# Performance work log

Measured on AMD Instinct MI355X. Metric: run time of the kernel, lower is better.

## Reference

```python
import jax, jax.numpy as jnp
import numpy as np

N_NODES = 50000


def _add_self_loops(src, dst, n):
    loop = jnp.arange(n, dtype=src.dtype)
    return jnp.concatenate([src, loop]), jnp.concatenate([dst, loop])


def gcn_conv(x, src, dst, W, b, n):
    # PyG GCNConv: out = D^-1/2 (A+I) D^-1/2 (x W) + b
    h = x @ W                                        # [N, out]
    deg = jnp.zeros((n,), h.dtype).at[dst].add(1.0)  # in-degree incl. self-loops
    dinv = jax.lax.rsqrt(jnp.maximum(deg, 1e-12))
    norm = dinv[src] * dinv[dst]                     # [E]
    msg = h[src] * norm[:, None]                     # [E, out] gather
    return jax.ops.segment_sum(msg, dst, num_segments=n) + b


def setup_inputs() -> dict:
    key = jax.random.key(0)
    ks = jax.random.split(key, 10)
    num_features, hidden = 256, 64
    x = jax.random.normal(ks[0], (N_NODES, num_features), jnp.float32)
    edge_index = jax.random.randint(ks[1], (2, 1600000), 0, N_NODES, jnp.int64)

    def glorot(k, fi, fo):
        s = jnp.sqrt(6.0 / (fi + fo)).astype(jnp.float32)
        return jax.random.uniform(k, (fi, fo), jnp.float32, -s, s)

    dims = [(num_features, 2 * hidden), (2 * hidden, hidden),
            (hidden, 2 * hidden), (2 * hidden, num_features)]
    params = {}
    for i, (fi, fo) in enumerate(dims):
        params[f"W{i+1}"] = glorot(ks[2 + i], fi, fo)
        params[f"b{i+1}"] = jnp.zeros((fo,), jnp.float32)
    return {"x": x, "edge_index": edge_index, **params}


def reference(x, edge_index, W1, b1, W2, b2, W3, b3, W4, b4):
    n = x.shape[0]
    src, dst = _add_self_loops(edge_index[0], edge_index[1], n)
    h = jax.nn.relu(gcn_conv(x, src, dst, W1, b1, n))
    z = jax.nn.relu(gcn_conv(h, src, dst, W2, b2, n))
    h = jax.nn.relu(gcn_conv(z, src, dst, W3, b3, n))
    x_hat = gcn_conv(h, src, dst, W4, b4, n)
    return x_hat
```

## Files before the change

### kernel.cpp

```cpp
#include <hip/hip_runtime.h>
#include <cstdint>
#include <cstddef>


static inline int cdiv(int a, int b) { return (a + b - 1) / b; }

typedef _Float16 half8v __attribute__((ext_vector_type(8)));
typedef float f32x4 __attribute__((ext_vector_type(4)));

#define NBMAX 784
#define SCHUNK 8192

__global__ __launch_bounds__(256) void k_bhist(const int* __restrict__ dst,
                                               int* __restrict__ bh,
                                               int E, int nb, int perBlock) {
  __shared__ int h[NBMAX];
  for (int i = threadIdx.x; i < nb; i += 256) h[i] = 0;
  __syncthreads();
  int beg = blockIdx.x * perBlock;
  int end = min(beg + perBlock, E);
  for (int e = beg + threadIdx.x; e < end; e += 256)
    atomicAdd(&h[dst[e] >> 6], 1);
  __syncthreads();
  for (int i = threadIdx.x; i < nb; i += 256)
    if (h[i]) atomicAdd(&bh[i], h[i]);
}

__global__ __launch_bounds__(256) void k_bscan(const int* __restrict__ bh,
                                               int* __restrict__ boff,
                                               int* __restrict__ bcur, int nb) {
  __shared__ int tsum[256];
  int t = threadIdx.x;
  int v[4];
  int s = 0;
#pragma unroll
  for (int i = 0; i < 4; ++i) {
    int idx = t * 4 + i;
    v[i] = (idx < nb) ? bh[idx] : 0;
    s += v[i];
  }
  tsum[t] = s;
  __syncthreads();
  int x = s;
  for (int d = 1; d < 256; d <<= 1) {
    int add = (t >= d) ? tsum[t - d] : 0;
    __syncthreads();
    x += add;
    tsum[t] = x;
    __syncthreads();
  }
  int base = x - s;
#pragma unroll
  for (int i = 0; i < 4; ++i) {
    int idx = t * 4 + i;
    if (idx < nb) { boff[idx] = base; bcur[idx] = base; }
    base += v[i];
  }
  if (t == 255) boff[nb] = base;
}

__global__ __launch_bounds__(256) void k_bscatter(const int* __restrict__ src,
                                                  const int* __restrict__ dst,
                                                  int* __restrict__ bcur,
                                                  unsigned* __restrict__ tmp,
                                                  int E, int nb) {
  __shared__ int hist[NBMAX];
  __shared__ int base[NBMAX];
  int beg = blockIdx.x * SCHUNK;
  int end = min(beg + SCHUNK, E);
  for (int i = threadIdx.x; i < nb; i += 256) hist[i] = 0;
  __syncthreads();
  for (int e = beg + threadIdx.x; e < end; e += 256)
    atomicAdd(&hist[dst[e] >> 6], 1);
  __syncthreads();
  for (int b = threadIdx.x; b < nb; b += 256) {
    int c = hist[b];
    base[b] = c ? atomicAdd(&bcur[b], c) : 0;
    hist[b] = 0;
  }
  __syncthreads();
  for (int e = beg + threadIdx.x; e < end; e += 256) {
    int d = dst[e];
    int b = d >> 6;
    int lp = atomicAdd(&hist[b], 1);
    tmp[base[b] + lp] = ((unsigned)(d & 63) << 16) | (unsigned)src[e];
  }
}

__global__ __launch_bounds__(256) void k_bsort(const unsigned* __restrict__ tmp,
                                               const int* __restrict__ boff,
                                               unsigned short* __restrict__ esrc,
                                               int* __restrict__ offs,
                                               int* __restrict__ counts,
                                               float* __restrict__ dinv,
                                               int N) {
  __shared__ int hist[64], cur[64];
  int b = blockIdx.x;
  int t = threadIdx.x;
  if (t < 64) hist[t] = 0;
  __syncthreads();
  int beg = boff[b], end = boff[b + 1];
  int cnt = end - beg;
  for (int i = t; i < cnt; i += 256) atomicAdd(&hist[tmp[beg + i] >> 16], 1);
  __syncthreads();
  if (t < 64) {
    int v = hist[t];
    int x = v;
#pragma unroll
    for (int d = 1; d < 64; d <<= 1) {
      int up = __shfl_up(x, d, 64);
      if (t >= d) x += up;
    }
    int ex = x - v;
    cur[t] = ex;
    int node = b * 64 + t;
    if (node < N) {
      counts[node] = v;
      offs[node] = beg + ex;
      dinv[node] = rsqrtf((float)(v + 1));
    }
  }
  __syncthreads();
  for (int i = t; i < cnt; i += 256) {
    unsigned v = tmp[beg + i];
    int pos = atomicAdd(&cur[v >> 16], 1);
    esrc[beg + pos] = (unsigned short)(v & 0xFFFFu);
  }
}

__global__ __launch_bounds__(256) void k_prepw(const float* __restrict__ W1,
                                               const float* __restrict__ W2,
                                               const float* __restrict__ W3,
                                               const float* __restrict__ W4,
                                               _Float16* __restrict__ W1t,
                                               _Float16* __restrict__ W2t,
                                               _Float16* __restrict__ W3t,
                                               _Float16* __restrict__ W4t,
                                               int* __restrict__ bh) {
  int t = blockIdx.x * 256 + threadIdx.x;
  if (t < NBMAX) bh[t] = 0;
  if (t < 32768) {
    int m = t >> 8, k = t & 255;
    W1t[t] = (_Float16)W1[k * 128 + m];
  } else if (t < 40960) {
    int u = t - 32768;
    int m = u >> 7, k = u & 127;
    W2t[u] = (_Float16)W2[k * 64 + m];
  } else if (t < 49152) {
    int u = t - 40960;
    int m = u >> 6, k = u & 63;
    W3t[u] = (_Float16)W3[k * 128 + m];
  } else if (t < 81920) {
    int u = t - 49152;
    int m = u >> 7, k = u & 127;
    W4t[u] = (_Float16)W4[k * 256 + m];
  }
}

template <int W, int BIAS, int RELU, int POST>
__global__ __launch_bounds__(256) void k_pull16(const _Float16* __restrict__ h,
                                                const unsigned short* __restrict__ esrc,
                                                const int* __restrict__ offs,
                                                const int* __restrict__ counts,
                                                const float* __restrict__ dinv,
                                                const float* __restrict__ bias,
                                                _Float16* __restrict__ out, int n) {
  const int LPR = W / 8;
  const int GRP = 64 / LPR;
  int node = blockIdx.x * 4 + (threadIdx.x >> 6);
  if (node >= n) return;
  int lane = threadIdx.x & 63;
  int g  = lane / LPR;
  int fl = lane % LPR;
  size_t rbase = (size_t)node * W + fl * 8;

  float acc[8] = {};
  if (g == 0) {
    half8v sv = *(const half8v*)&h[rbase];
#pragma unroll
    for (int q = 0; q < 8; ++q) acc[q] = (float)sv[q];
  }

  int beg = offs[node];
  int cnt = counts[node];
  int j = g;
  for (; j + 3 * GRP < cnt; j += 4 * GRP) {
    int s0 = esrc[beg + j];
    int s1 = esrc[beg + j + GRP];
    int s2 = esrc[beg + j + 2 * GRP];
    int s3 = esrc[beg + j + 3 * GRP];
    half8v v0 = *(const half8v*)&h[(size_t)s0 * W + fl * 8];
    half8v v1 = *(const half8v*)&h[(size_t)s1 * W + fl * 8];
    half8v v2 = *(const half8v*)&h[(size_t)s2 * W + fl * 8];
    half8v v3 = *(const half8v*)&h[(size_t)s3 * W + fl * 8];
#pragma unroll
    for (int q = 0; q < 8; ++q)
      acc[q] += ((float)v0[q] + (float)v1[q]) + ((float)v2[q] + (float)v3[q]);
  }
  for (; j < cnt; j += GRP) {
    int s = esrc[beg + j];
    half8v v = *(const half8v*)&h[(size_t)s * W + fl * 8];
#pragma unroll
    for (int q = 0; q < 8; ++q) acc[q] += (float)v[q];
  }

#pragma unroll
  for (int d = LPR; d < 64; d <<= 1) {
#pragma unroll
    for (int q = 0; q < 8; ++q) acc[q] += __shfl_xor(acc[q], d, 64);
  }

  if (g == 0) {
    float dv = dinv[node];
    float t[8];
#pragma unroll
    for (int q = 0; q < 8; ++q) t[q] = dv * acc[q];
    if (BIAS) {
#pragma unroll
      for (int q = 0; q < 8; ++q) t[q] += bias[fl * 8 + q];
    }
    if (RELU) {
#pragma unroll
      for (int q = 0; q < 8; ++q) t[q] = fmaxf(t[q], 0.f);
    }
    if (POST) {
#pragma unroll
      for (int q = 0; q < 8; ++q) t[q] *= dv;
    }
    half8v o;
#pragma unroll
    for (int q = 0; q < 8; ++q) o[q] = (_Float16)t[q];
    *(half8v*)&out[rbase] = o;
  }
}

template <int M, int K, int BIAS, int RELU, int SCALE, int AF32, int OUTF16>
__global__ __launch_bounds__(256) void k_gemm_mfma(const void* __restrict__ Av,
                                                   const _Float16* __restrict__ Wt,
                                                   const float* __restrict__ bias,
                                                   const float* __restrict__ dinv,
                                                   void* __restrict__ Cv, int N) {
  const int NT = M / 64;
  const int ST = K / 32;
  const int w  = threadIdx.x >> 6;
  const int l  = threadIdx.x & 63;
  const int lr = l & 15;
  const int lk = l >> 4;
  const int r0 = blockIdx.x * 16;
  int arow = r0 + lr;
  if (arow >= N) arow = N - 1;

  half8v a_all[ST];
  half8v b_all[ST][NT];

#pragma unroll
  for (int s = 0; s < ST; ++s) {
    int k0 = s * 32;
    if (AF32) {
      const float* ap = &((const float*)Av)[(size_t)arow * K + k0 + lk * 8];
      float4 f0 = *(const float4*)ap;
      float4 f1 = *(const float4*)(ap + 4);
      half8v a;
      a[0] = (_Float16)f0.x; a[1] = (_Float16)f0.y;
      a[2] = (_Float16)f0.z; a[3] = (_Float16)f0.w;
      a[4] = (_Float16)f1.x; a[5] = (_Float16)f1.y;
      a[6] = (_Float16)f1.z; a[7] = (_Float16)f1.w;
      a_all[s] = a;
    } else {
      a_all[s] = *(const half8v*)&((const _Float16*)Av)[(size_t)arow * K + k0 + lk * 8];
    }
#pragma unroll
    for (int ct = 0; ct < NT; ++ct) {
      int col0 = (w * NT + ct) * 16;
      b_all[s][ct] = *(const half8v*)&Wt[(size_t)(col0 + lr) * K + k0 + lk * 8];
    }
  }

  f32x4 acc[NT] = {};
#pragma unroll
  for (int s = 0; s < ST; ++s)
#pragma unroll
    for (int ct = 0; ct < NT; ++ct)
      acc[ct] = __builtin_amdgcn_mfma_f32_16x16x32_f16(a_all[s], b_all[s][ct], acc[ct], 0, 0, 0);

  float dvv[4];
  int okr[4];
#pragma unroll
  for (int r = 0; r < 4; ++r) {
    int ro = r0 + lk * 4 + r;
    okr[r] = (ro < N);
    dvv[r] = (SCALE && okr[r]) ? dinv[ro] : 1.0f;
  }
#pragma unroll
  for (int ct = 0; ct < NT; ++ct) {
    int col = (w * NT + ct) * 16 + lr;
    float bs = BIAS ? bias[col] : 0.f;
#pragma unroll
    for (int r = 0; r < 4; ++r) {
      if (!okr[r]) continue;
      int ro = r0 + lk * 4 + r;
      float v = acc[ct][r] + bs;
      if (RELU) v = fmaxf(v, 0.f);
      if (SCALE) v *= dvv[r];
      if (OUTF16) ((_Float16*)Cv)[(size_t)ro * M + col] = (_Float16)v;
      else        ((float*)Cv)[(size_t)ro * M + col] = v;
    }
  }
}

extern "C" void kernel_launch(void* const* d_in, const int* in_sizes, int n_in,
                              void* d_out, int out_size, void* d_ws, size_t ws_size,
                              hipStream_t stream) {
  const float* x  = (const float*)d_in[0];
  const int*   ei = (const int*)d_in[1];
  const float* W1 = (const float*)d_in[2];
  const float* b1 = (const float*)d_in[3];
  const float* W2 = (const float*)d_in[4];
  const float* b2 = (const float*)d_in[5];
  const float* W3 = (const float*)d_in[6];
  const float* b3 = (const float*)d_in[7];
  const float* W4 = (const float*)d_in[8];
  const float* b4 = (const float*)d_in[9];

  const int N = in_sizes[0] / 256;
  const int E = in_sizes[1] / 2;
  const int* src = ei;
  const int* dst = ei + E;
  const int nb = cdiv(N, 64);

  const int NP = 50176;
  int*   bh     = (int*)d_ws;
  int*   boff   = bh + NBMAX;
  int*   bcur   = boff + NBMAX;
  int*   counts = bcur + NBMAX;
  int*   offs   = counts + NP;
  float* dinv   = (float*)(offs + NP);
  unsigned short* esrc = (unsigned short*)(dinv + NP);
  _Float16* W1t = (_Float16*)(esrc + E);
  _Float16* W2t = W1t + 32768;
  _Float16* W3t = W2t + 8192;
  _Float16* W4t = W3t + 8192;
  _Float16* bufA = (_Float16*)(((uintptr_t)(W4t + 32768) + 255) & ~(uintptr_t)255);
  _Float16* bufB = bufA + (size_t)N * 128;
  _Float16* bufC = bufB + (size_t)N * 128;
  _Float16* bufD = bufC + (size_t)N * 64;
  unsigned* tmp = (unsigned*)bufA;
  float* out = (float*)d_out;

  dim3 blk(256);

  k_prepw<<<320, blk, 0, stream>>>(W1, W2, W3, W4, W1t, W2t, W3t, W4t, bh);
  {
    int nblk = 256;
    int perBlock = cdiv(E, nblk);
    k_bhist<<<nblk, blk, 0, stream>>>(dst, bh, E, nb, perBlock);
  }
  k_bscan<<<1, blk, 0, stream>>>(bh, boff, bcur, nb);
  k_bscatter<<<cdiv(E, SCHUNK), blk, 0, stream>>>(src, dst, bcur, tmp, E, nb);
  k_bsort<<<nb, blk, 0, stream>>>(tmp, boff, esrc, offs, counts, dinv, N);

  dim3 gpull(cdiv(N, 4));
  dim3 ggemm(cdiv(N, 16));

  k_gemm_mfma<128, 256, 0, 0, 1, 1, 1><<<ggemm, blk, 0, stream>>>(x, W1t, nullptr, dinv, bufA, N);
  k_pull16<128, 1, 1, 0><<<gpull, blk, 0, stream>>>(bufA, esrc, offs, counts, dinv, b1, bufB, N);
  k_gemm_mfma<64, 128, 0, 0, 1, 0, 1><<<ggemm, blk, 0, stream>>>(bufB, W2t, nullptr, dinv, bufC, N);
  k_pull16<64, 1, 1, 1><<<gpull, blk, 0, stream>>>(bufC, esrc, offs, counts, dinv, b2, bufD, N);
  k_pull16<64, 0, 0, 0><<<gpull, blk, 0, stream>>>(bufD, esrc, offs, counts, dinv, nullptr, bufC, N);
  k_gemm_mfma<128, 64, 1, 1, 1, 0, 1><<<ggemm, blk, 0, stream>>>(bufC, W3t, b3, dinv, bufA, N);
  k_pull16<128, 0, 0, 0><<<gpull, blk, 0, stream>>>(bufA, esrc, offs, counts, dinv, nullptr, bufB, N);
  k_gemm_mfma<256, 128, 1, 0, 0, 0, 0><<<ggemm, blk, 0, stream>>>(bufB, W4t, b4, nullptr, out, N);
}
```

Before: 340.0 us.

## Stage 64-row A tiles in LDS to reuse register-held weights across rows

The MFMA GEMM now processes 64 rows per block instead of 16. It stages the A tile in padded shared memory and loops over four 16-row sub-tiles while keeping the weight fragments in registers. This amortizes the weight loads, which were previously reloaded from global/L2 for every 16 rows, over four times as many rows. In exchange it adds LDS usage (up to about 33 KB for K=256), a block barrier, and a quarter as many blocks, which could reduce occupancy and latency hiding.

```diff
diff --git a/kernel.cpp b/kernel.cpp
--- a/kernel.cpp
+++ b/kernel.cpp
@@ -242,68 +242,81 @@
                                                    void* __restrict__ Cv, int N) {
   const int NT = M / 64;
   const int ST = K / 32;
-  const int w  = threadIdx.x >> 6;
-  const int l  = threadIdx.x & 63;
+  const int ROWW = K + 8;
+  __shared__ _Float16 Als[64 * ROWW];
+
+  const int tid = threadIdx.x;
+  const int r0 = blockIdx.x * 64;
+
+  const int CH = K / 8;
+  for (int i = tid; i < 64 * CH; i += 256) {
+    int r = i / CH, c = i % CH;
+    int gr = r0 + r;
+    if (gr >= N) gr = N - 1;
+    half8v v;
+    if (AF32) {
+      const float* ap = &((const float*)Av)[(size_t)gr * K + c * 8];
+      float4 f0 = *(const float4*)ap;
+      float4 f1 = *(const float4*)(ap + 4);
+      v[0] = (_Float16)f0.x; v[1] = (_Float16)f0.y;
+      v[2] = (_Float16)f0.z; v[3] = (_Float16)f0.w;
+      v[4] = (_Float16)f1.x; v[5] = (_Float16)f1.y;
+      v[6] = (_Float16)f1.z; v[7] = (_Float16)f1.w;
+    } else {
+      v = *(const half8v*)&((const _Float16*)Av)[(size_t)gr * K + c * 8];
+    }
+    *(half8v*)&Als[r * ROWW + c * 8] = v;
+  }
+
+  const int w  = tid >> 6;
+  const int l  = tid & 63;
   const int lr = l & 15;
   const int lk = l >> 4;
-  const int r0 = blockIdx.x * 16;
-  int arow = r0 + lr;
-  if (arow >= N) arow = N - 1;
-
-  half8v a_all[ST];
+
   half8v b_all[ST][NT];
-
-#pragma unroll
-  for (int s = 0; s < ST; ++s) {
-    int k0 = s * 32;
-    if (AF32) {
-      const float* ap = &((const float*)Av)[(size_t)arow * K + k0 + lk * 8];
-      float4 f0 = *(const float4*)ap;
-      float4 f1 = *(const float4*)(ap + 4);
-      half8v a;
-      a[0] = (_Float16)f0.x; a[1] = (_Float16)f0.y;
-      a[2] = (_Float16)f0.z; a[3] = (_Float16)f0.w;
-      a[4] = (_Float16)f1.x; a[5] = (_Float16)f1.y;
-      a[6] = (_Float16)f1.z; a[7] = (_Float16)f1.w;
-      a_all[s] = a;
-    } else {
-      a_all[s] = *(const half8v*)&((const _Float16*)Av)[(size_t)arow * K + k0 + lk * 8];
-    }
+#pragma unroll
+  for (int s = 0; s < ST; ++s)
 #pragma unroll
     for (int ct = 0; ct < NT; ++ct) {
       int col0 = (w * NT + ct) * 16;
-      b_all[s][ct] = *(const half8v*)&Wt[(size_t)(col0 + lr) * K + k0 + lk * 8];
-    }
-  }
-
-  f32x4 acc[NT] = {};
-#pragma unroll
-  for (int s = 0; s < ST; ++s)
-#pragma unroll
-    for (int ct = 0; ct < NT; ++ct)
-      acc[ct] = __builtin_amdgcn_mfma_f32_16x16x32_f16(a_all[s], b_all[s][ct], acc[ct], 0, 0, 0);
-
-  float dvv[4];
-  int okr[4];
-#pragma unroll
-  for (int r = 0; r < 4; ++r) {
-    int ro = r0 + lk * 4 + r;
-    okr[r] = (ro < N);
-    dvv[r] = (SCALE && okr[r]) ? dinv[ro] : 1.0f;
-  }
-#pragma unroll
-  for (int ct = 0; ct < NT; ++ct) {
-    int col = (w * NT + ct) * 16 + lr;
-    float bs = BIAS ? bias[col] : 0.f;
+      b_all[s][ct] = *(const half8v*)&Wt[(size_t)(col0 + lr) * K + s * 32 + lk * 8];
+    }
+
+  __syncthreads();
+
+  for (int rt = 0; rt < 4; ++rt) {
+    f32x4 acc[NT] = {};
+#pragma unroll
+    for (int s = 0; s < ST; ++s) {
+      half8v a = *(const half8v*)&Als[(rt * 16 + lr) * ROWW + s * 32 + lk * 8];
+#pragma unroll
+      for (int ct = 0; ct < NT; ++ct)
+        acc[ct] = __builtin_amdgcn_mfma_f32_16x16x32_f16(a, b_all[s][ct], acc[ct], 0, 0, 0);
+    }
+
+    int rbase = r0 + rt * 16;
+    float dvv[4];
+    int okr[4];
 #pragma unroll
     for (int r = 0; r < 4; ++r) {
-      if (!okr[r]) continue;
-      int ro = r0 + lk * 4 + r;
-      float v = acc[ct][r] + bs;
-      if (RELU) v = fmaxf(v, 0.f);
-      if (SCALE) v *= dvv[r];
-      if (OUTF16) ((_Float16*)Cv)[(size_t)ro * M + col] = (_Float16)v;
-      else        ((float*)Cv)[(size_t)ro * M + col] = v;
+      int ro = rbase + lk * 4 + r;
+      okr[r] = (ro < N);
+      dvv[r] = (SCALE && okr[r]) ? dinv[ro] : 1.0f;
+    }
+#pragma unroll
+    for (int ct = 0; ct < NT; ++ct) {
+      int col = (w * NT + ct) * 16 + lr;
+      float bs = BIAS ? bias[col] : 0.f;
+#pragma unroll
+      for (int r = 0; r < 4; ++r) {
+        if (!okr[r]) continue;
+        int ro = rbase + lk * 4 + r;
+        float v = acc[ct][r] + bs;
+        if (RELU) v = fmaxf(v, 0.f);
+        if (SCALE) v *= dvv[r];
+        if (OUTF16) ((_Float16*)Cv)[(size_t)ro * M + col] = (_Float16)v;
+        else        ((float*)Cv)[(size_t)ro * M + col] = v;
+      }
     }
   }
 }
@@ -360,7 +373,7 @@
   k_bsort<<<nb, blk, 0, stream>>>(tmp, boff, esrc, offs, counts, dinv, N);
 
   dim3 gpull(cdiv(N, 4));
-  dim3 ggemm(cdiv(N, 16));
+  dim3 ggemm(cdiv(N, 64));
 
   k_gemm_mfma<128, 256, 0, 0, 1, 1, 1><<<ggemm, blk, 0, stream>>>(x, W1t, nullptr, dinv, bufA, N);
   k_pull16<128, 1, 1, 0><<<gpull, blk, 0, stream>>>(bufA, esrc, offs, counts, dinv, b1, bufB, N);
```

Measured after the change: 287.9 us, median of 2. 15.3% less time.
